# Kernel tuning notes

Hardware: AMD Instinct MI355X
Metric: run time of the kernel (lower is better)

Reference implementation:

```python
import jax, jax.numpy as jnp
import numpy as np

_INF = 1e9  # large finite 'infinity' for squared distances (max real sq-dist ~ 3*47^2)


def _minplus_last(f):
    """Exact 1D squared Euclidean distance transform along the last axis:
    g[x] = min_j f[j] + (x - j)^2 (brute-force min-plus, fully vectorized)."""
    n = f.shape[-1]
    i = jnp.arange(n)
    d2 = ((i[:, None] - i[None, :]) ** 2).astype(f.dtype)  # (n_out, n_in)
    return jnp.min(f[..., None, :] + d2, axis=-1)


def _edt(src):
    """Exact Euclidean distance to the nearest True voxel of `src` over the last
    3 (spatial) axes. Equivalent to scipy.ndimage.distance_transform_edt(~src)
    (distance to nearest zero of ~src). Separable squared-distance passes."""
    f = jnp.where(src, 0.0, _INF).astype(jnp.float32)
    for ax in (-3, -2, -1):
        f = jnp.moveaxis(_minplus_last(jnp.moveaxis(f, ax, -1)), -1, ax)
    return jnp.sqrt(f)


def _signed_distance_maps(onehot):
    """onehot: (B, C, D, H, W) in {0,1}. Returns SDF = posdis - negdis per (b,c),
    zeroed where the class is absent in that batch element (matches torch code)."""
    pos = onehot.astype(bool)
    stacked = jnp.stack([pos, ~pos], axis=0)          # (2, B, C, D, H, W)
    dists = _edt(stacked)                              # exact EDT for both masks
    posdis, negdis = dists[0], dists[1]
    has_pos = pos.any(axis=(-3, -2, -1))               # (B, C)
    sdf = jnp.where(has_pos[..., None, None, None], posdis - negdis, 0.0)
    return sdf


def setup_inputs() -> dict:
    key = jax.random.key(0)
    k1, k2 = jax.random.split(key)
    B, C, D, H, W = 2, 4, 48, 48, 48
    pred = jax.random.normal(k1, (B, C, D, H, W), dtype=jnp.float32)
    target = jax.random.randint(k2, (B, D, H, W), 0, C, dtype=jnp.int64)
    return {"pred": pred, "target": target}


def reference(pred, target):
    num_classes = pred.shape[1]
    # one-hot encode target: (B, C, D, H, W)
    onehot = (target[:, None] == jnp.arange(num_classes)[None, :, None, None, None])
    onehot = onehot.astype(jnp.float32)
    pred_softmax = jax.nn.softmax(pred, axis=1)
    sdf = _signed_distance_maps(onehot)                # no-grad quantity
    return jnp.mean(jnp.abs(pred_softmax * sdf))
```

## Files before the change

### kernel.cpp

```cpp
#include <hip/hip_runtime.h>
#include <hip/hip_bf16.h>


#define SPATIAL 110592
#define NB 2
#define NC 4
#define NLINE 48
#define SLABP 49

__global__ __launch_bounds__(192) void edt_wh_kernel(const int* __restrict__ target,
                                                     float* __restrict__ F,
                                                     float* __restrict__ out) {
    __shared__ float slab[NLINE * SLABP];
    int blk = blockIdx.x;
    int vol = blk / NLINE, d = blk - vol * NLINE;
    int mask = vol >> 3;
    int b = (vol >> 2) & 1, c = vol & 3;
    int tid = threadIdx.x;
    if (blk == 0 && tid == 0) *out = 0.0f;

    const int* tslab = target + (b * NLINE + d) * (NLINE * NLINE);
    for (int idx = tid; idx < NLINE * NLINE; idx += 192) {
        int h = idx / NLINE, w = idx - h * NLINE;
        bool pos = (tslab[idx] == c);
        bool set = mask ? !pos : pos;
        slab[h * SLABP + w] = set ? 0.0f : 1e9f;
    }
    __syncthreads();

    {
        int h = tid >> 2, cx = (tid & 3) * 12;
        float m[12];
#pragma unroll
        for (int k = 0; k < 12; ++k) m[k] = 1e30f;
        float x0 = (float)cx;
        for (int j = 0; j < NLINE; ++j) {
            float fj = slab[h * SLABP + j];
            float dj = x0 - (float)j;
#pragma unroll
            for (int k = 0; k < 12; ++k) {
                float dd = dj + (float)k;
                m[k] = fminf(m[k], fmaf(dd, dd, fj));
            }
        }
        __syncthreads();
#pragma unroll
        for (int k = 0; k < 12; ++k) slab[h * SLABP + cx + k] = m[k];
        __syncthreads();
    }

    {
        int w = tid >> 2, cx = (tid & 3) * 12;
        float m[12];
#pragma unroll
        for (int k = 0; k < 12; ++k) m[k] = 1e30f;
        float x0 = (float)cx;
        for (int j = 0; j < NLINE; ++j) {
            float fj = slab[j * SLABP + w];
            float dj = x0 - (float)j;
#pragma unroll
            for (int k = 0; k < 12; ++k) {
                float dd = dj + (float)k;
                m[k] = fminf(m[k], fmaf(dd, dd, fj));
            }
        }
        __syncthreads();
#pragma unroll
        for (int k = 0; k < 12; ++k) slab[(cx + k) * SLABP + w] = m[k];
        __syncthreads();
    }

    float* fvol = F + (long)vol * SPATIAL + (long)d * (NLINE * NLINE);
    for (int idx = tid; idx < NLINE * NLINE; idx += 192) {
        int h = idx / NLINE, w = idx - h * NLINE;
        fvol[idx] = slab[h * SLABP + w];
    }
}

__global__ __launch_bounds__(192) void edt_d_reduce_kernel(const float* __restrict__ pred,
                                                           const float* __restrict__ F,
                                                           float* __restrict__ out) {
    __shared__ float slabP[NLINE * SLABP];
    __shared__ float slabN[NLINE * SLABP];
    int blk = blockIdx.x;
    int bc = blk / NLINE, h = blk - bc * NLINE;
    int b = bc >> 2, c = bc & 3;
    int tid = threadIdx.x;

    const float* fp = F + (long)bc * SPATIAL;
    const float* fn = F + (long)(8 + bc) * SPATIAL;
    for (int idx = tid; idx < NLINE * NLINE; idx += 192) {
        int dd = idx / NLINE, w = idx - dd * NLINE;
        long g = (long)dd * (NLINE * NLINE) + h * NLINE + w;
        slabP[dd * SLABP + w] = fp[g];
        slabN[dd * SLABP + w] = fn[g];
    }
    __syncthreads();

    int w = tid >> 2, cx = (tid & 3) * 12;
    float mP[12], mN[12];
#pragma unroll
    for (int k = 0; k < 12; ++k) { mP[k] = 1e30f; mN[k] = 1e30f; }
    float x0 = (float)cx;
    for (int j = 0; j < NLINE; ++j) {
        float fpj = slabP[j * SLABP + w];
        float fnj = slabN[j * SLABP + w];
        float dj = x0 - (float)j;
#pragma unroll
        for (int k = 0; k < 12; ++k) {
            float dd = dj + (float)k;
            float q = dd * dd;
            mP[k] = fminf(mP[k], q + fpj);
            mN[k] = fminf(mN[k], q + fnj);
        }
    }

    float acc = 0.0f;
    long pbase = (long)b * NC * SPATIAL + (long)h * NLINE + w;
#pragma unroll 4
    for (int k = 0; k < 12; ++k) {
        int d = cx + k;
        float psq = mP[k], nsq = mN[k];
        float sdf = (psq > 1e8f) ? 0.0f : (sqrtf(psq) - sqrtf(nsq));
        long base = pbase + (long)d * (NLINE * NLINE);
        float p0 = pred[base];
        float p1 = pred[base + SPATIAL];
        float p2 = pred[base + 2 * SPATIAL];
        float p3 = pred[base + 3 * SPATIAL];
        float mx = fmaxf(fmaxf(p0, p1), fmaxf(p2, p3));
        float e0 = __expf(p0 - mx), e1 = __expf(p1 - mx);
        float e2 = __expf(p2 - mx), e3 = __expf(p3 - mx);
        float sum = e0 + e1 + e2 + e3;
        float ec = (c == 0) ? e0 : (c == 1) ? e1 : (c == 2) ? e2 : e3;
        acc += (ec / sum) * fabsf(sdf);
    }

#pragma unroll
    for (int o = 32; o > 0; o >>= 1) acc += __shfl_down(acc, o, 64);
    __shared__ float wpart[3];
    int lane = tid & 63, wid = tid >> 6;
    if (lane == 0) wpart[wid] = acc;
    __syncthreads();
    if (tid == 0) {
        float v = wpart[0] + wpart[1] + wpart[2];
        atomicAdd(out, v * (1.0f / (float)(NB * NC * SPATIAL)));
    }
}

extern "C" void kernel_launch(void* const* d_in, const int* in_sizes, int n_in,
                              void* d_out, int out_size, void* d_ws, size_t ws_size,
                              hipStream_t stream) {
    const float* pred = (const float*)d_in[0];
    const int* target = (const int*)d_in[1];
    float* out = (float*)d_out;
    float* F = (float*)d_ws;

    edt_wh_kernel<<<2 * NB * NC * NLINE, 192, 0, stream>>>(target, F, out);
    edt_d_reduce_kernel<<<NB * NC * NLINE, 192, 0, stream>>>(pred, F, out);
}
```

Baseline: 101.7 us.

## Expand squared distance algebraically and split depth pass across two blocks

The inner min-plus loops now compute (dj+k)^2+f as (dj^2+f) + 2k*dj, so each candidate costs one FMA plus a min, and the constant k^2 term is added once at the end. The depth pass with the fused reduction launches twice as many blocks, each handling half of the output depths with 6 accumulators per thread instead of 12. This is meant to raise parallelism and cut register pressure in the second kernel. The cost is that each half-block reloads the full P/N slabs, doubling that global read traffic, and the expanded form slightly changes float rounding for large values.

After: 94.38 us. 1.08x faster.

```diff
diff --git a/kernel.cpp b/kernel.cpp
--- a/kernel.cpp
+++ b/kernel.cpp
@@ -33,19 +33,19 @@
         float m[12];
 #pragma unroll
         for (int k = 0; k < 12; ++k) m[k] = 1e30f;
-        float x0 = (float)cx;
+        float dj = (float)cx;
         for (int j = 0; j < NLINE; ++j) {
             float fj = slab[h * SLABP + j];
-            float dj = x0 - (float)j;
+            float aj = fmaf(dj, dj, fj);
 #pragma unroll
-            for (int k = 0; k < 12; ++k) {
-                float dd = dj + (float)k;
-                m[k] = fminf(m[k], fmaf(dd, dd, fj));
-            }
+            for (int k = 0; k < 12; ++k)
+                m[k] = fminf(m[k], fmaf((float)(2 * k), dj, aj));
+            dj -= 1.0f;
         }
         __syncthreads();
 #pragma unroll
-        for (int k = 0; k < 12; ++k) slab[h * SLABP + cx + k] = m[k];
+        for (int k = 0; k < 12; ++k)
+            slab[h * SLABP + cx + k] = m[k] + (float)(k * k);
         __syncthreads();
     }
 
@@ -54,19 +54,19 @@
         float m[12];
 #pragma unroll
         for (int k = 0; k < 12; ++k) m[k] = 1e30f;
-        float x0 = (float)cx;
+        float dj = (float)cx;
         for (int j = 0; j < NLINE; ++j) {
             float fj = slab[j * SLABP + w];
-            float dj = x0 - (float)j;
+            float aj = fmaf(dj, dj, fj);
 #pragma unroll
-            for (int k = 0; k < 12; ++k) {
-                float dd = dj + (float)k;
-                m[k] = fminf(m[k], fmaf(dd, dd, fj));
-            }
+            for (int k = 0; k < 12; ++k)
+                m[k] = fminf(m[k], fmaf((float)(2 * k), dj, aj));
+            dj -= 1.0f;
         }
         __syncthreads();
 #pragma unroll
-        for (int k = 0; k < 12; ++k) slab[(cx + k) * SLABP + w] = m[k];
+        for (int k = 0; k < 12; ++k)
+            slab[(cx + k) * SLABP + w] = m[k] + (float)(k * k);
         __syncthreads();
     }
 
@@ -83,7 +83,9 @@
     __shared__ float slabP[NLINE * SLABP];
     __shared__ float slabN[NLINE * SLABP];
     int blk = blockIdx.x;
-    int bc = blk / NLINE, h = blk - bc * NLINE;
+    int half = blk & 1;
+    int rest = blk >> 1;
+    int bc = rest / NLINE, h = rest - bc * NLINE;
     int b = bc >> 2, c = bc & 3;
     int tid = threadIdx.x;
 
@@ -97,30 +99,33 @@
     }
     __syncthreads();
 
-    int w = tid >> 2, cx = (tid & 3) * 12;
-    float mP[12], mN[12];
+    int w = tid >> 2;
+    int cx = half * 24 + (tid & 3) * 6;
+    float mP[6], mN[6];
 #pragma unroll
-    for (int k = 0; k < 12; ++k) { mP[k] = 1e30f; mN[k] = 1e30f; }
-    float x0 = (float)cx;
+    for (int k = 0; k < 6; ++k) { mP[k] = 1e30f; mN[k] = 1e30f; }
+    float dj = (float)cx;
     for (int j = 0; j < NLINE; ++j) {
         float fpj = slabP[j * SLABP + w];
         float fnj = slabN[j * SLABP + w];
-        float dj = x0 - (float)j;
+        float aP = fmaf(dj, dj, fpj);
+        float aN = fmaf(dj, dj, fnj);
 #pragma unroll
-        for (int k = 0; k < 12; ++k) {
-            float dd = dj + (float)k;
-            float q = dd * dd;
-            mP[k] = fminf(mP[k], q + fpj);
-            mN[k] = fminf(mN[k], q + fnj);
+        for (int k = 0; k < 6; ++k) {
+            float tk = (float)(2 * k);
+            mP[k] = fminf(mP[k], fmaf(tk, dj, aP));
+            mN[k] = fminf(mN[k], fmaf(tk, dj, aN));
         }
+        dj -= 1.0f;
     }
 
     float acc = 0.0f;
     long pbase = (long)b * NC * SPATIAL + (long)h * NLINE + w;
-#pragma unroll 4
-    for (int k = 0; k < 12; ++k) {
+#pragma unroll
+    for (int k = 0; k < 6; ++k) {
         int d = cx + k;
-        float psq = mP[k], nsq = mN[k];
+        float psq = mP[k] + (float)(k * k);
+        float nsq = mN[k] + (float)(k * k);
         float sdf = (psq > 1e8f) ? 0.0f : (sqrtf(psq) - sqrtf(nsq));
         long base = pbase + (long)d * (NLINE * NLINE);
         float p0 = pred[base];
@@ -156,5 +161,5 @@
     float* F = (float*)d_ws;
 
     edt_wh_kernel<<<2 * NB * NC * NLINE, 192, 0, stream>>>(target, F, out);
-    edt_d_reduce_kernel<<<NB * NC * NLINE, 192, 0, stream>>>(pred, F, out);
+    edt_d_reduce_kernel<<<2 * NB * NC * NLINE, 192, 0, stream>>>(pred, F, out);
 }
```
